# Kernel tuning notes

Measured on AMD Instinct MI355X. Metric: run time of the kernel, lower is better.

The kernel has to match this reference:

```python
import jax, jax.numpy as jnp
import numpy as np

N_NODES, N_EDGES = 16000, 256000
M_IN_S, M_IN_V = 16, 8   # input irreps: 16x0e + 8x1o (dim 40)
M_K_S, M_K_V = 8, 4      # key/query irreps: 8x0e + 4x1o
M_V_S, M_V_V = 16, 8     # value irreps: 16x0e + 8x1o
NUM_BASIS, R_CUT = 32, 2.5
SQ3 = 1.7320508075688772  # sqrt(3)


def _fc_net(r, W1, W2):
    # e3nn FullyConnectedNet([num_basis,16,numels], silu): weight-normalized linears
    h = jax.nn.silu(r @ (W1 / jnp.sqrt(jnp.float32(W1.shape[0]))))
    return h @ (W2 / jnp.sqrt(jnp.float32(W2.shape[0])))


def _edge_tp(xs, xv, y0, y1, w, m1s, m1v, mos, mov):
    # FullyConnectedTensorProduct(in1 = m1s x0e + m1v x1o, in2 = 1x0e + 1x1o,
    #   out = mos x0e + mov x1o), per-edge external weights w [E, numels].
    # Paths: 0e*0e->0e, 1o*1o->0e (dot/sqrt3), 0e*1o->1o, 1o*0e->1o.
    E = w.shape[0]
    n1, n2, n3 = m1s * mos, m1v * mos, m1s * mov
    w_ss = w[:, :n1].reshape(E, m1s, mos)
    w_vv = w[:, n1:n1 + n2].reshape(E, m1v, mos)
    w_sv = w[:, n1 + n2:n1 + n2 + n3].reshape(E, m1s, mov)
    w_vs = w[:, n1 + n2 + n3:].reshape(E, m1v, mov)
    inv = 1.0 / jnp.sqrt(jnp.float32(m1s + m1v))  # fan-in path normalization
    out_s = (jnp.einsum('ei,eio->eo', xs * y0[:, None], w_ss)
             + jnp.einsum('eic,ec,eio->eo', xv, y1, w_vv) / SQ3) * inv
    out_v = (jnp.einsum('ei,ec,eio->eoc', xs, y1, w_sv)
             + jnp.einsum('eic,eio->eoc', xv * y0[:, None, None], w_vs)) * inv
    return out_s, out_v


def _forward(pos, x, Wq_s, Wq_v, Wk1, Wk2, Wv1, Wv2, Ws_ss, Ws_vv, edge_src, edge_dst):
    xs, xv = x[:, :M_IN_S], x[:, M_IN_S:].reshape(-1, M_IN_V, 3)
    vec = pos[edge_dst] - pos[edge_src]                       # [E,3]
    d = jnp.linalg.norm(vec, axis=1)
    d_safe = jnp.maximum(d, 1e-6)
    # bessel radial basis with cutoff (soft_one_hot_linspace, basis='bessel') * sqrt(num_basis)
    n = jnp.arange(1, NUM_BASIS + 1, dtype=jnp.float32)
    rad = jnp.sqrt(2.0 / R_CUT) * jnp.sin(n[None] * jnp.pi * d_safe[:, None] / R_CUT) / d_safe[:, None]
    rad = jnp.where((d < R_CUT)[:, None], rad, 0.0) * jnp.sqrt(jnp.float32(NUM_BASIS))
    # spherical harmonics lmax=1, normalize=True, component normalization
    vh = vec / d_safe[:, None]
    y0, y1 = jnp.ones_like(d), SQ3 * vh
    # query projection (o3.Linear: per-irrep linear with 1/sqrt(fan_in))
    q_s = xs @ Wq_s / jnp.sqrt(jnp.float32(M_IN_S))           # [N, M_K_S]
    q_v = jnp.einsum('nic,io->noc', xv, Wq_v) / jnp.sqrt(jnp.float32(M_IN_V))
    # per-edge tensor-product weights from radial MLPs (shared_weights=False)
    wk = _fc_net(rad, Wk1, Wk2)                               # [E, 288]
    wv = _fc_net(rad, Wv1, Wv2)                               # [E, 576]
    xs_e, xv_e = xs[edge_src], xv[edge_src]
    k_s, k_v = _edge_tp(xs_e, xv_e, y0, y1, wk, M_IN_S, M_IN_V, M_K_S, M_K_V)
    v_s, v_v = _edge_tp(xs_e, xv_e, y0, y1, wv, M_IN_S, M_IN_V, M_V_S, M_V_V)
    # similarity tensor product (query x key -> 0e), shared internal weights
    fan = jnp.sqrt(jnp.float32(M_K_S * M_K_S + M_K_V * M_K_V))
    sim = (jnp.einsum('ei,ij,ej->e', q_s[edge_dst], Ws_ss, k_s)
           + jnp.einsum('eic,ij,ejc->e', q_v[edge_dst], Ws_vv, k_v) / SQ3) / fan
    # scatter softmax over incoming edges of each dst node
    attn = jnp.exp(sim)
    Z = jax.ops.segment_sum(attn, edge_dst, num_segments=N_NODES)
    a = attn / Z[edge_dst]
    # weighted scatter-sum aggregation
    out_s = jax.ops.segment_sum(a[:, None] * v_s, edge_dst, num_segments=N_NODES)
    out_v = jax.ops.segment_sum(a[:, None, None] * v_v, edge_dst, num_segments=N_NODES)
    return jnp.concatenate([out_s, out_v.reshape(N_NODES, -1)], axis=1)  # [N, 40]


def setup_inputs() -> dict:
    key = jax.random.key(0)
    ks = jax.random.split(key, 12)
    wk_numels = M_IN_S * M_K_S + M_IN_V * M_K_S + M_IN_S * M_K_V + M_IN_V * M_K_V  # 288
    wv_numels = M_IN_S * M_V_S + M_IN_V * M_V_S + M_IN_S * M_V_V + M_IN_V * M_V_V  # 576
    return {
        'pos': jax.random.uniform(ks[0], (N_NODES, 3), jnp.float32) * 3.0,
        'x': jax.random.normal(ks[1], (N_NODES, M_IN_S + 3 * M_IN_V), jnp.float32),
        'Wq_s': jax.random.normal(ks[2], (M_IN_S, M_K_S), jnp.float32),
        'Wq_v': jax.random.normal(ks[3], (M_IN_V, M_K_V), jnp.float32),
        'Wk1': jax.random.normal(ks[4], (NUM_BASIS, 16), jnp.float32),
        'Wk2': jax.random.normal(ks[5], (16, wk_numels), jnp.float32),
        'Wv1': jax.random.normal(ks[6], (NUM_BASIS, 16), jnp.float32),
        'Wv2': jax.random.normal(ks[7], (16, wv_numels), jnp.float32),
        'Ws_ss': jax.random.normal(ks[8], (M_K_S, M_K_S), jnp.float32) * 0.1,
        'Ws_vv': jax.random.normal(ks[9], (M_K_V, M_K_V), jnp.float32) * 0.1,
        'edge_src': jax.random.randint(ks[10], (N_EDGES,), 0, N_NODES),
        'edge_dst': jax.random.randint(ks[11], (N_EDGES,), 0, N_NODES),
    }


def reference(pos, x, Wq_s, Wq_v, Wk1, Wk2, Wv1, Wv2, Ws_ss, Ws_vv, edge_src, edge_dst):
    return _forward(pos, x, Wq_s, Wq_v, Wk1, Wk2, Wv1, Wv2, Ws_ss, Ws_vv, edge_src, edge_dst)
```

## Files before the change

kernel.cpp:

```cpp
#include <hip/hip_runtime.h>
#include <hip/hip_bf16.h>

#define N_NODES 16000
#define N_EDGES 256000

#define OFF_SD     0
#define OFF_SIMB   512000
#define OFF_CNT    768000
#define OFF_START  784000
#define OFF_CUR    800001
#define OFF_WB     816004
#define OFF_WBK    834436

typedef _Float16 f16x2 __attribute__((ext_vector_type(2)));
typedef _Float16 f16x8v __attribute__((ext_vector_type(8)));
typedef float f32x4v __attribute__((ext_vector_type(4)));

__device__ __forceinline__ float fdot2f(f16x2 a, f16x2 b, float c) {
#if __has_builtin(__builtin_amdgcn_fdot2)
  return __builtin_amdgcn_fdot2(a, b, c, false);
#else
  return fmaf((float)a.x, (float)b.x, fmaf((float)a.y, (float)b.y, c));
#endif
}

__device__ __forceinline__ unsigned packh2(float a, float b) {
  union { unsigned u; f16x2 p; } v;
  v.p.x = (_Float16)a; v.p.y = (_Float16)b;
  return v.u;
}

__device__ __forceinline__ void load_row40(const float* __restrict__ p, float* xr) {
  const float4* rp = reinterpret_cast<const float4*>(p);
#pragma unroll
  for (int q = 0; q < 10; ++q) {
    float4 f = rp[q];
    xr[4 * q + 0] = f.x; xr[4 * q + 1] = f.y; xr[4 * q + 2] = f.z; xr[4 * q + 3] = f.w;
  }
}

struct EdgeGeom { float vhx, vhy, vhz, y1x, y1y, y1z; };

__device__ __forceinline__ void edge_h_pk(const float* __restrict__ pos, int s, int d,
                                          const unsigned* W1, f16x2* hp, EdgeGeom& g) {
  float vx = pos[3 * d + 0] - pos[3 * s + 0];
  float vy = pos[3 * d + 1] - pos[3 * s + 1];
  float vz = pos[3 * d + 2] - pos[3 * s + 2];
  float dist = sqrtf(fmaf(vx, vx, fmaf(vy, vy, vz * vz)));
  float dsafe = fmaxf(dist, 1e-6f);
  float rinv = 1.0f / dsafe;
  g.vhx = vx * rinv; g.vhy = vy * rinv; g.vhz = vz * rinv;
  g.y1x = 1.7320508075688772f * g.vhx;
  g.y1y = 1.7320508075688772f * g.vhy;
  g.y1z = 1.7320508075688772f * g.vhz;
  float pre[16];
#pragma unroll
  for (int t = 0; t < 16; ++t) pre[t] = 0.f;
  float sx, cx;
  sincosf(1.2566370614359172f * dsafe, &sx, &cx);
  cx = fminf(1.f, fmaxf(-1.f, cx));
  float twoc = 2.f * cx;
  float sprev = 0.f, scur = sx;
  float rscale = (dist < 2.5f) ? (5.059644256269407f * rinv) : 0.f;
#pragma unroll
  for (int bp = 0; bp < 16; ++bp) {
    float r0 = rscale * scur;
    float sn = fmaf(twoc, scur, -sprev); sprev = scur; scur = sn;
    float r1 = rscale * scur;
    sn = fmaf(twoc, scur, -sprev); sprev = scur; scur = sn;
    union { unsigned u; f16x2 p; } rp; rp.p.x = (_Float16)r0; rp.p.y = (_Float16)r1;
    union { uint4 u[4]; f16x2 p[16]; } w;
    w.u[0] = *(const uint4*)(W1 + bp * 16);
    w.u[1] = *(const uint4*)(W1 + bp * 16 + 4);
    w.u[2] = *(const uint4*)(W1 + bp * 16 + 8);
    w.u[3] = *(const uint4*)(W1 + bp * 16 + 12);
#pragma unroll
    for (int t = 0; t < 16; ++t) pre[t] = fdot2f(rp.p, w.p[t], pre[t]);
  }
#pragma unroll
  for (int tp = 0; tp < 8; ++tp) {
    float h0 = pre[2 * tp]     / (1.f + __expf(-pre[2 * tp]));
    float h1 = pre[2 * tp + 1] / (1.f + __expf(-pre[2 * tp + 1]));
    hp[tp].x = (_Float16)h0; hp[tp].y = (_Float16)h1;
  }
}

__global__ void k_hist(const int* __restrict__ edst, int* __restrict__ cnt) {
  int e = blockIdx.x * 256 + threadIdx.x;
  atomicAdd(&cnt[edst[e]], 1);
}

__global__ void __launch_bounds__(1024) k_scan(const int* __restrict__ cnt,
                                               int* __restrict__ start, int* __restrict__ cur) {
  __shared__ int part[1024];
  int t = threadIdx.x;
  int base = t * 16;
  int local[16];
  int sum = 0;
#pragma unroll
  for (int i = 0; i < 16; ++i) {
    int idx = base + i;
    int c = (idx < N_NODES) ? cnt[idx] : 0;
    local[i] = sum; sum += c;
  }
  part[t] = sum;
  __syncthreads();
  for (int off = 1; off < 1024; off <<= 1) {
    int v = (t >= off) ? part[t - off] : 0;
    __syncthreads();
    part[t] += v;
    __syncthreads();
  }
  int prev = (t == 0) ? 0 : part[t - 1];
#pragma unroll
  for (int i = 0; i < 16; ++i) {
    int idx = base + i;
    if (idx < N_NODES) { int st = prev + local[i]; start[idx] = st; cur[idx] = st; }
  }
  if (t == 0) start[N_NODES] = N_EDGES;
}

__global__ void k_fill(const int* __restrict__ esrc, const int* __restrict__ edst,
                       int* __restrict__ cur, int2* __restrict__ sd) {
  int e = blockIdx.x * 256 + threadIdx.x;
  int d = edst[e];
  int slot = atomicAdd(&cur[d], 1);
  sd[slot] = make_int2(esrc[e], d);
}

__global__ void k_prepB(const float* __restrict__ Wv2, unsigned short* __restrict__ WB) {
  int idx = blockIdx.x * 256 + threadIdx.x;
  int j = idx & 7;
  int lane = (idx >> 3) & 63;
  int t3 = idx >> 9;
  int ct = t3 % 3, kk = t3 / 3;
  int q = lane >> 4, m = lane & 15;
  int row = 32 * kk + 8 * q + j;
  int col = 16 * ct + m;
  int t = row & 15;
  float v = 0.f;
  if (row < 256) {
    int i = row >> 4;
    if (col < 16)      v = Wv2[t * 576 + i * 16 + col];
    else if (col < 24) v = Wv2[t * 576 + 384 + i * 8 + (col - 16)];
  } else if (row < 384) {
    int i = (row - 256) >> 4;
    if (col < 16)      v = Wv2[t * 576 + 256 + i * 16 + col];
  } else {
    int part = (row - 384) >> 7;
    int i = ((row - 384) & 127) >> 4;
    int cb = 24 + 8 * part;
    if (col >= cb && col < cb + 8) v = Wv2[t * 576 + 512 + i * 8 + (col - cb)];
  }
  union { unsigned short u; _Float16 h; } cv;
  cv.h = (_Float16)(v * 0.051031036307982884f);
  WB[idx] = cv.u;
}

__global__ void k_prepBK(const float* __restrict__ Wk2, unsigned short* __restrict__ WBK) {
  int idx = blockIdx.x * 256 + threadIdx.x;
  int j = idx & 7;
  int lane = (idx >> 3) & 63;
  int t2 = idx >> 9;
  int ct = t2 & 1, kk = t2 >> 1;
  int q = lane >> 4, m = lane & 15;
  int row = 32 * kk + 8 * q + j;
  int col = 16 * ct + m;
  int t = row & 15;
  float v = 0.f;
  if (col < 24) {
    if (row < 256) {
      int i = row >> 4;
      if (col < 8)       v = Wk2[t * 288 + i * 8 + col];
      else if (col < 12) v = Wk2[t * 288 + 192 + i * 4 + (col - 8)];
    } else if (row < 384) {
      int i = (row - 256) >> 4;
      if (col < 8)       v = Wk2[t * 288 + 128 + i * 8 + col];
    } else {
      int c = (row - 384) >> 7;
      int i = ((row - 384) & 127) >> 4;
      int cb = 12 + 4 * c;
      if (col >= cb && col < cb + 4) v = Wk2[t * 288 + 256 + i * 4 + (col - cb)];
    }
  }
  union { unsigned short u; _Float16 h; } cv;
  cv.h = (_Float16)(v * 0.051031036307982884f);
  WBK[idx] = cv.u;
}

#define ZTW 20

__global__ void __launch_bounds__(256) k_edge1(
    const float* __restrict__ pos, const float* __restrict__ x,
    const float* __restrict__ Wq_s, const float* __restrict__ Wq_v,
    const float* __restrict__ Wk1,
    const float* __restrict__ Wss, const float* __restrict__ Wvv,
    const unsigned short* __restrict__ WBK,
    const int2* __restrict__ sd, float* __restrict__ simb) {
  __shared__ __align__(16) unsigned LW1[256];
  __shared__ float Ls[240];
  __shared__ __align__(16) float SM[4][64 * ZTW];

  for (int i = threadIdx.x; i < 256; i += 256) {
    int bp = i >> 4, t = i & 15;
    LW1[i] = packh2(Wk1[(2 * bp) * 16 + t] * 0.17677669529663687f,
                    Wk1[(2 * bp + 1) * 16 + t] * 0.17677669529663687f);
  }
  for (int i = threadIdx.x; i < 240; i += 256) {
    float v;
    if (i < 128)      v = Wq_s[i] * 0.25f;
    else if (i < 160) v = Wq_v[i - 128] * 0.3535533905932738f;
    else if (i < 224) v = Wss[i - 160] * 0.11180339887498948f;
    else              v = Wvv[i - 224] * 0.06454972243679028f;
    Ls[i] = v;
  }
  __syncthreads();

  int wave = threadIdx.x >> 6, lane = threadIdx.x & 63;
  int q = lane >> 4, m = lane & 15;
  int slot = blockIdx.x * 256 + threadIdx.x;
  int2 e = sd[slot];
  int s = e.x, d = e.y;

  f16x2 hp[8]; EdgeGeom g;
  edge_h_pk(pos, s, d, LW1, hp, g);

  float qts[8], qtv[12];
  {
    float xd[40];
    load_row40(x + 40 * d, xd);
    float qd[8], qvd[12];
#pragma unroll
    for (int o = 0; o < 8; ++o) qd[o] = 0.f;
#pragma unroll
    for (int i = 0; i < 16; ++i)
#pragma unroll
      for (int o = 0; o < 8; ++o) qd[o] = fmaf(xd[i], Ls[8 * i + o], qd[o]);
#pragma unroll
    for (int k = 0; k < 12; ++k) qvd[k] = 0.f;
#pragma unroll
    for (int i = 0; i < 8; ++i)
#pragma unroll
      for (int o = 0; o < 4; ++o)
#pragma unroll
        for (int c = 0; c < 3; ++c)
          qvd[3 * o + c] = fmaf(xd[16 + 3 * i + c], Ls[128 + 4 * i + o], qvd[3 * o + c]);
#pragma unroll
    for (int j = 0; j < 8; ++j) {
      float t = 0.f;
#pragma unroll
      for (int i = 0; i < 8; ++i) t = fmaf(qd[i], Ls[160 + 8 * i + j], t);
      qts[j] = t;
    }
#pragma unroll
    for (int o = 0; o < 4; ++o)
#pragma unroll
      for (int c = 0; c < 3; ++c) {
        float t = 0.f;
#pragma unroll
        for (int i = 0; i < 4; ++i) t = fmaf(qvd[3 * i + c], Ls[224 + 4 * i + o], t);
        qtv[3 * o + c] = t;
      }
  }

  float xr[40];
  load_row40(x + 40 * s, xr);
  float xs[16];
#pragma unroll
  for (int i = 0; i < 16; ++i) xs[i] = xr[i];
  float Bv[8];
#pragma unroll
  for (int i = 0; i < 8; ++i)
    Bv[i] = fmaf(xr[16 + 3 * i], g.vhx, fmaf(xr[17 + 3 * i], g.vhy, xr[18 + 3 * i] * g.vhz));
  f16x2 cxv[3][4];
#pragma unroll
  for (int p = 0; p < 4; ++p)
#pragma unroll
    for (int c = 0; c < 3; ++c) {
      cxv[c][p].x = (_Float16)xr[16 + 3 * (2 * p) + c];
      cxv[c][p].y = (_Float16)xr[16 + 3 * (2 * p + 1) + c];
    }

  unsigned* zt = (unsigned*)&SM[wave][0];
  const uint4* WBq = (const uint4*)WBK;
  f32x4v acc[4][2];
#pragma unroll
  for (int rt = 0; rt < 4; ++rt)
#pragma unroll
    for (int ct = 0; ct < 2; ++ct) { f32x4v z = {0.f, 0.f, 0.f, 0.f}; acc[rt][ct] = z; }

#pragma unroll
  for (int kk = 0; kk < 24; ++kk) {
    f16x2 sp0, sp1;
    if (kk < 8) {
      sp0.x = sp0.y = (_Float16)xs[2 * kk];
      sp1.x = sp1.y = (_Float16)xs[2 * kk + 1];
    } else if (kk < 12) {
      sp0.x = sp0.y = (_Float16)Bv[2 * (kk - 8)];
      sp1.x = sp1.y = (_Float16)Bv[2 * (kk - 8) + 1];
    } else {
      int part = (kk - 12) >> 2, p = (kk - 12) & 3;
      sp0.x = sp0.y = cxv[part][p].x;
      sp1.x = sp1.y = cxv[part][p].y;
    }
    union { uint4 u[4]; f16x2 z[16]; } Z;
#pragma unroll
    for (int t = 0; t < 8; ++t) { Z.z[t] = hp[t] * sp0; Z.z[8 + t] = hp[t] * sp1; }
    uint4* zrow = (uint4*)(zt + lane * ZTW);
    zrow[0] = Z.u[0]; zrow[1] = Z.u[1]; zrow[2] = Z.u[2]; zrow[3] = Z.u[3];
    union { uint4 u; f16x8v v; } af[4];
#pragma unroll
    for (int rt = 0; rt < 4; ++rt)
      af[rt].u = *(const uint4*)(zt + (16 * rt + m) * ZTW + 4 * q);
#pragma unroll
    for (int ct = 0; ct < 2; ++ct) {
      union { uint4 u; f16x8v v; } bf;
      bf.u = WBq[(kk * 2 + ct) * 64 + lane];
#pragma unroll
      for (int rt = 0; rt < 4; ++rt)
        acc[rt][ct] = __builtin_amdgcn_mfma_f32_16x16x32_f16(af[rt].v, bf.v, acc[rt][ct], 0, 0, 0);
    }
  }

  float P[24];
  float* ctb = &SM[wave][0];
#pragma unroll
  for (int rt = 0; rt < 4; ++rt)
#pragma unroll
    for (int r = 0; r < 4; ++r)
      ctb[(16 * rt + 4 * q + r) * ZTW + m] = acc[rt][0][r];
#pragma unroll
  for (int b = 0; b < 4; ++b) {
    float4 f = *(const float4*)(ctb + lane * ZTW + 4 * b);
    P[4 * b] = f.x; P[4 * b + 1] = f.y; P[4 * b + 2] = f.z; P[4 * b + 3] = f.w;
  }
#pragma unroll
  for (int rt = 0; rt < 4; ++rt)
#pragma unroll
    for (int r = 0; r < 4; ++r)
      ctb[(16 * rt + 4 * q + r) * ZTW + m] = acc[rt][1][r];
#pragma unroll
  for (int b = 0; b < 2; ++b) {
    float4 f = *(const float4*)(ctb + lane * ZTW + 4 * b);
    P[16 + 4 * b] = f.x; P[17 + 4 * b] = f.y; P[18 + 4 * b] = f.z; P[19 + 4 * b] = f.w;
  }

  float sim = 0.f;
#pragma unroll
  for (int j = 0; j < 8; ++j) sim = fmaf(qts[j], P[j], sim);
  float y1c[3] = {g.y1x, g.y1y, g.y1z};
#pragma unroll
  for (int o = 0; o < 4; ++o)
#pragma unroll
    for (int c = 0; c < 3; ++c)
      sim = fmaf(qtv[3 * o + c], fmaf(y1c[c], P[8 + o], P[12 + 4 * c + o]), sim);
  simb[slot] = sim;
}

__global__ void k_norm(const int* __restrict__ start, float* __restrict__ simb) {
  int n = blockIdx.x * 256 + threadIdx.x;
  if (n >= N_NODES) return;
  int a = start[n], b = start[n + 1];
  if (a == b) return;
  float m = -3.4e38f;
  for (int j = a; j < b; ++j) m = fmaxf(m, simb[j]);
  float Z = 0.f;
  for (int j = a; j < b; ++j) { float t = __expf(simb[j] - m); simb[j] = t; Z += t; }
  float inv = 1.f / Z;
  for (int j = a; j < b; ++j) simb[j] *= inv;
}

__global__ void __launch_bounds__(256) k_edge2(
    const float* __restrict__ pos, const float* __restrict__ x,
    const float* __restrict__ Wv1, const unsigned short* __restrict__ WB,
    const int2* __restrict__ sd, const float* __restrict__ ab, float* __restrict__ out) {
  __shared__ __align__(16) unsigned LW1[256];
  __shared__ __align__(16) float SM[4][64 * ZTW];

  for (int i = threadIdx.x; i < 256; i += 256) {
    int bp = i >> 4, t = i & 15;
    LW1[i] = packh2(Wv1[(2 * bp) * 16 + t] * 0.17677669529663687f,
                    Wv1[(2 * bp + 1) * 16 + t] * 0.17677669529663687f);
  }
  __syncthreads();

  int wave = threadIdx.x >> 6, lane = threadIdx.x & 63;
  int q = lane >> 4, m = lane & 15;
  int slot = blockIdx.x * 256 + threadIdx.x;
  int2 e = sd[slot];
  int s = e.x, d = e.y;

  bool same[6];
#pragma unroll
  for (int k = 0; k < 6; ++k) {
    int dd = __shfl_down(d, 1 << k, 64);
    same[k] = ((lane + (1 << k)) < 64) && (dd == d);
  }
  int dprev = __shfl_up(d, 1, 64);
  bool head = (lane == 0) || (dprev != d);

  f16x2 hp[8]; EdgeGeom g;
  edge_h_pk(pos, s, d, LW1, hp, g);
  float xr[40];
  load_row40(x + 40 * s, xr);
  float xs[16];
#pragma unroll
  for (int i = 0; i < 16; ++i) xs[i] = xr[i];
  float Bv[8];
#pragma unroll
  for (int i = 0; i < 8; ++i)
    Bv[i] = fmaf(xr[16 + 3 * i], g.vhx, fmaf(xr[17 + 3 * i], g.vhy, xr[18 + 3 * i] * g.vhz));
  f16x2 cxv[3][4];
#pragma unroll
  for (int p = 0; p < 4; ++p)
#pragma unroll
    for (int c = 0; c < 3; ++c) {
      cxv[c][p].x = (_Float16)xr[16 + 3 * (2 * p) + c];
      cxv[c][p].y = (_Float16)xr[16 + 3 * (2 * p + 1) + c];
    }
  float a = ab[slot];

  unsigned* zt = (unsigned*)&SM[wave][0];
  const uint4* WBq = (const uint4*)WB;
  f32x4v acc[4][3];
#pragma unroll
  for (int rt = 0; rt < 4; ++rt)
#pragma unroll
    for (int ct = 0; ct < 3; ++ct) { f32x4v z = {0.f, 0.f, 0.f, 0.f}; acc[rt][ct] = z; }

#pragma unroll
  for (int kk = 0; kk < 24; ++kk) {
    f16x2 sp0, sp1;
    if (kk < 8) {
      sp0.x = sp0.y = (_Float16)xs[2 * kk];
      sp1.x = sp1.y = (_Float16)xs[2 * kk + 1];
    } else if (kk < 12) {
      sp0.x = sp0.y = (_Float16)Bv[2 * (kk - 8)];
      sp1.x = sp1.y = (_Float16)Bv[2 * (kk - 8) + 1];
    } else {
      int part = (kk - 12) >> 2, p = (kk - 12) & 3;
      sp0.x = sp0.y = cxv[part][p].x;
      sp1.x = sp1.y = cxv[part][p].y;
    }
    union { uint4 u[4]; f16x2 z[16]; } Z;
#pragma unroll
    for (int t = 0; t < 8; ++t) { Z.z[t] = hp[t] * sp0; Z.z[8 + t] = hp[t] * sp1; }
    uint4* zrow = (uint4*)(zt + lane * ZTW);
    zrow[0] = Z.u[0]; zrow[1] = Z.u[1]; zrow[2] = Z.u[2]; zrow[3] = Z.u[3];
    union { uint4 u; f16x8v v; } af[4];
#pragma unroll
    for (int rt = 0; rt < 4; ++rt)
      af[rt].u = *(const uint4*)(zt + (16 * rt + m) * ZTW + 4 * q);
#pragma unroll
    for (int ct = 0; ct < 3; ++ct) {
      union { uint4 u; f16x8v v; } bf;
      bf.u = WBq[(kk * 3 + ct) * 64 + lane];
#pragma unroll
      for (int rt = 0; rt < 4; ++rt)
        acc[rt][ct] = __builtin_amdgcn_mfma_f32_16x16x32_f16(af[rt].v, bf.v, acc[rt][ct], 0, 0, 0);
    }
  }

  float* ctb = &SM[wave][0];
  float* op = out + 40 * d;

  {
#pragma unroll
    for (int rt = 0; rt < 4; ++rt)
#pragma unroll
      for (int r = 0; r < 4; ++r)
        ctb[(16 * rt + 4 * q + r) * ZTW + m] = acc[rt][0][r];
    float P0[16];
#pragma unroll
    for (int b = 0; b < 4; ++b) {
      float4 f = *(const float4*)(ctb + lane * ZTW + 4 * b);
      P0[4 * b] = f.x; P0[4 * b + 1] = f.y; P0[4 * b + 2] = f.z; P0[4 * b + 3] = f.w;
    }
#pragma unroll
    for (int o = 0; o < 16; ++o) {
      float v = a * P0[o];
#pragma unroll
      for (int k = 0; k < 6; ++k) {
        float ov = __shfl_down(v, 1 << k, 64);
        v += same[k] ? ov : 0.f;
      }
      if (head) atomicAdd(op + o, v);
    }
  }
  float P1[16], P2[16];
#pragma unroll
  for (int rt = 0; rt < 4; ++rt)
#pragma unroll
    for (int r = 0; r < 4; ++r)
      ctb[(16 * rt + 4 * q + r) * ZTW + m] = acc[rt][1][r];
#pragma unroll
  for (int b = 0; b < 4; ++b) {
    float4 f = *(const float4*)(ctb + lane * ZTW + 4 * b);
    P1[4 * b] = f.x; P1[4 * b + 1] = f.y; P1[4 * b + 2] = f.z; P1[4 * b + 3] = f.w;
  }
#pragma unroll
  for (int rt = 0; rt < 4; ++rt)
#pragma unroll
    for (int r = 0; r < 4; ++r)
      ctb[(16 * rt + 4 * q + r) * ZTW + m] = acc[rt][2][r];
#pragma unroll
  for (int b = 0; b < 4; ++b) {
    float4 f = *(const float4*)(ctb + lane * ZTW + 4 * b);
    P2[4 * b] = f.x; P2[4 * b + 1] = f.y; P2[4 * b + 2] = f.z; P2[4 * b + 3] = f.w;
  }
#pragma unroll
  for (int o = 0; o < 8; ++o) {
    float s1v = P1[o];
    float vc[3];
    vc[0] = a * fmaf(g.y1x, s1v, P1[8 + o]);
    vc[1] = a * fmaf(g.y1y, s1v, P2[o]);
    vc[2] = a * fmaf(g.y1z, s1v, P2[8 + o]);
#pragma unroll
    for (int c = 0; c < 3; ++c) {
      float v = vc[c];
#pragma unroll
      for (int k = 0; k < 6; ++k) {
        float ov = __shfl_down(v, 1 << k, 64);
        v += same[k] ? ov : 0.f;
      }
      if (head) atomicAdd(op + 16 + 3 * o + c, v);
    }
  }
}

extern "C" void kernel_launch(void* const* d_in, const int* in_sizes, int n_in,
                              void* d_out, int out_size, void* d_ws, size_t ws_size,
                              hipStream_t stream) {
  (void)in_sizes; (void)n_in; (void)out_size; (void)ws_size;
  const float* pos  = (const float*)d_in[0];
  const float* x    = (const float*)d_in[1];
  const float* Wq_s = (const float*)d_in[2];
  const float* Wq_v = (const float*)d_in[3];
  const float* Wk1  = (const float*)d_in[4];
  const float* Wk2  = (const float*)d_in[5];
  const float* Wv1  = (const float*)d_in[6];
  const float* Wv2  = (const float*)d_in[7];
  const float* Wss  = (const float*)d_in[8];
  const float* Wvv  = (const float*)d_in[9];
  const int* esrc = (const int*)d_in[10];
  const int* edst = (const int*)d_in[11];
  int*   wsi  = (int*)d_ws;
  float* wsf  = (float*)d_ws;
  float* out  = (float*)d_out;

  int2*  sd    = (int2*)(wsi + OFF_SD);
  float* simb  = wsf + OFF_SIMB;
  int*   cnt   = wsi + OFF_CNT;
  int*   start = wsi + OFF_START;
  int*   cur   = wsi + OFF_CUR;
  unsigned short* WB  = (unsigned short*)(wsf + OFF_WB);
  unsigned short* WBK = (unsigned short*)(wsf + OFF_WBK);

  hipMemsetAsync(cnt, 0, (size_t)N_NODES * sizeof(int), stream);
  hipMemsetAsync(out, 0, (size_t)(N_NODES * 40) * sizeof(float), stream);
  k_prepB<<<144, 256, 0, stream>>>(Wv2, WB);
  k_prepBK<<<96, 256, 0, stream>>>(Wk2, WBK);
  k_hist<<<1000, 256, 0, stream>>>(edst, cnt);
  k_scan<<<1, 1024, 0, stream>>>(cnt, start, cur);
  k_fill<<<1000, 256, 0, stream>>>(esrc, edst, cur, sd);
  k_edge1<<<1000, 256, 0, stream>>>(pos, x, Wq_s, Wq_v, Wk1, Wss, Wvv, WBK, sd, simb);
  k_norm<<<63, 256, 0, stream>>>(start, simb);
  k_edge2<<<1000, 256, 0, stream>>>(pos, x, Wv1, WB, sd, simb, out);
}
```

Baseline: 247.2 us.

## Precompute per-node queries and build MFMA A-operands in registers via splat

Moves the query projection (Wq then Ws) out of the per-edge kernel into a new per-node kernel that writes fp16 queries, so each edge only loads 20 halves instead of recomputing from the 40-float destination row. The per-edge outer-product operand is now built in registers: h and the coefficients are staged once in LDS, and each k-step multiplies the h fragment by a perm-splatted coefficient. This replaces the per-k-step LDS write and readback. The C-tile transpose uses a padded stride-65 layout. Queries are now held in fp16, which costs some precision, and an extra small kernel launch is added.

New measurement: 236.8 us. -4.2%, faster.

```diff
diff --git a/kernel.cpp b/kernel.cpp
--- a/kernel.cpp
+++ b/kernel.cpp
@@ -11,6 +11,7 @@
 #define OFF_CUR    800001
 #define OFF_WB     816004
 #define OFF_WBK    834436
+#define OFF_QT     846724
 
 typedef _Float16 f16x2 __attribute__((ext_vector_type(2)));
 typedef _Float16 f16x8v __attribute__((ext_vector_type(8)));
@@ -28,6 +29,15 @@
   union { unsigned u; f16x2 p; } v;
   v.p.x = (_Float16)a; v.p.y = (_Float16)b;
   return v.u;
+}
+
+__device__ __forceinline__ unsigned splat_half(unsigned x, unsigned sel) {
+#if __has_builtin(__builtin_amdgcn_perm)
+  return __builtin_amdgcn_perm(x, x, sel);
+#else
+  unsigned h = (sel == 0x03020302u) ? (x >> 16) : (x & 0xffffu);
+  return h | (h << 16);
+#endif
 }
 
 __device__ __forceinline__ void load_row40(const float* __restrict__ p, float* xr) {
@@ -188,25 +198,13 @@
   WBK[idx] = cv.u;
 }
 
-#define ZTW 20
-
-__global__ void __launch_bounds__(256) k_edge1(
-    const float* __restrict__ pos, const float* __restrict__ x,
+__global__ void __launch_bounds__(128) k_nodeq(
+    const float* __restrict__ x,
     const float* __restrict__ Wq_s, const float* __restrict__ Wq_v,
-    const float* __restrict__ Wk1,
     const float* __restrict__ Wss, const float* __restrict__ Wvv,
-    const unsigned short* __restrict__ WBK,
-    const int2* __restrict__ sd, float* __restrict__ simb) {
-  __shared__ __align__(16) unsigned LW1[256];
+    unsigned short* __restrict__ QT) {
   __shared__ float Ls[240];
-  __shared__ __align__(16) float SM[4][64 * ZTW];
-
-  for (int i = threadIdx.x; i < 256; i += 256) {
-    int bp = i >> 4, t = i & 15;
-    LW1[i] = packh2(Wk1[(2 * bp) * 16 + t] * 0.17677669529663687f,
-                    Wk1[(2 * bp + 1) * 16 + t] * 0.17677669529663687f);
-  }
-  for (int i = threadIdx.x; i < 240; i += 256) {
+  for (int i = threadIdx.x; i < 240; i += 128) {
     float v;
     if (i < 128)      v = Wq_s[i] * 0.25f;
     else if (i < 160) v = Wq_v[i - 128] * 0.3535533905932738f;
@@ -215,9 +213,87 @@
     Ls[i] = v;
   }
   __syncthreads();
+  int n = blockIdx.x * 128 + threadIdx.x;
+  float xd[40];
+  load_row40(x + 40 * n, xd);
+  float qd[8], qvd[12];
+#pragma unroll
+  for (int o = 0; o < 8; ++o) qd[o] = 0.f;
+#pragma unroll
+  for (int i = 0; i < 16; ++i)
+#pragma unroll
+    for (int o = 0; o < 8; ++o) qd[o] = fmaf(xd[i], Ls[8 * i + o], qd[o]);
+#pragma unroll
+  for (int k = 0; k < 12; ++k) qvd[k] = 0.f;
+#pragma unroll
+  for (int i = 0; i < 8; ++i)
+#pragma unroll
+    for (int o = 0; o < 4; ++o)
+#pragma unroll
+      for (int c = 0; c < 3; ++c)
+        qvd[3 * o + c] = fmaf(xd[16 + 3 * i + c], Ls[128 + 4 * i + o], qvd[3 * o + c]);
+  float qf[20];
+#pragma unroll
+  for (int j = 0; j < 8; ++j) {
+    float t = 0.f;
+#pragma unroll
+    for (int i = 0; i < 8; ++i) t = fmaf(qd[i], Ls[160 + 8 * i + j], t);
+    qf[j] = t;
+  }
+#pragma unroll
+  for (int o = 0; o < 4; ++o)
+#pragma unroll
+    for (int c = 0; c < 3; ++c) {
+      float t = 0.f;
+#pragma unroll
+      for (int i = 0; i < 4; ++i) t = fmaf(qvd[3 * i + c], Ls[224 + 4 * i + o], t);
+      qf[8 + 3 * o + c] = t;
+    }
+  uint2* qp = (uint2*)(QT + 20 * n);
+#pragma unroll
+  for (int b = 0; b < 5; ++b) {
+    uint2 st;
+    st.x = packh2(qf[4 * b], qf[4 * b + 1]);
+    st.y = packh2(qf[4 * b + 2], qf[4 * b + 3]);
+    qp[b] = st;
+  }
+}
+
+#define RSTR 36
+
+__device__ __forceinline__ void build_coef(const float* xr, const float* Bv, float* coef) {
+#pragma unroll
+  for (int i = 0; i < 16; ++i) coef[i] = xr[i];
+#pragma unroll
+  for (int i = 0; i < 8; ++i) coef[16 + i] = Bv[i];
+#pragma unroll
+  for (int p = 0; p < 4; ++p)
+#pragma unroll
+    for (int c = 0; c < 3; ++c) {
+      coef[24 + 8 * c + 2 * p]     = xr[16 + 6 * p + c];
+      coef[24 + 8 * c + 2 * p + 1] = xr[16 + 6 * p + 3 + c];
+    }
+}
+
+__global__ void __launch_bounds__(256) k_edge1(
+    const float* __restrict__ pos, const float* __restrict__ x,
+    const float* __restrict__ Wk1, const unsigned short* __restrict__ WBK,
+    const unsigned short* __restrict__ QT,
+    const int2* __restrict__ sd, float* __restrict__ simb) {
+  __shared__ __align__(16) unsigned LW1[256];
+  __shared__ __align__(16) unsigned SM[4][64 * RSTR];
+
+  for (int i = threadIdx.x; i < 256; i += 256) {
+    int bp = i >> 4, t = i & 15;
+    LW1[i] = packh2(Wk1[(2 * bp) * 16 + t] * 0.17677669529663687f,
+                    Wk1[(2 * bp + 1) * 16 + t] * 0.17677669529663687f);
+  }
+  __syncthreads();
 
   int wave = threadIdx.x >> 6, lane = threadIdx.x & 63;
   int q = lane >> 4, m = lane & 15;
+  int q1 = q & 1;
+  unsigned seld = (q >> 1) ? 0x03020302u : 0x01000100u;
   int slot = blockIdx.x * 256 + threadIdx.x;
   int2 e = sd[slot];
   int s = e.x, d = e.y;
@@ -225,63 +301,51 @@
   f16x2 hp[8]; EdgeGeom g;
   edge_h_pk(pos, s, d, LW1, hp, g);
 
-  float qts[8], qtv[12];
+  float qf[20];
   {
-    float xd[40];
-    load_row40(x + 40 * d, xd);
-    float qd[8], qvd[12];
-#pragma unroll
-    for (int o = 0; o < 8; ++o) qd[o] = 0.f;
-#pragma unroll
-    for (int i = 0; i < 16; ++i)
-#pragma unroll
-      for (int o = 0; o < 8; ++o) qd[o] = fmaf(xd[i], Ls[8 * i + o], qd[o]);
-#pragma unroll
-    for (int k = 0; k < 12; ++k) qvd[k] = 0.f;
-#pragma unroll
-    for (int i = 0; i < 8; ++i)
-#pragma unroll
-      for (int o = 0; o < 4; ++o)
-#pragma unroll
-        for (int c = 0; c < 3; ++c)
-          qvd[3 * o + c] = fmaf(xd[16 + 3 * i + c], Ls[128 + 4 * i + o], qvd[3 * o + c]);
-#pragma unroll
-    for (int j = 0; j < 8; ++j) {
-      float t = 0.f;
-#pragma unroll
-      for (int i = 0; i < 8; ++i) t = fmaf(qd[i], Ls[160 + 8 * i + j], t);
-      qts[j] = t;
-    }
-#pragma unroll
-    for (int o = 0; o < 4; ++o)
-#pragma unroll
-      for (int c = 0; c < 3; ++c) {
-        float t = 0.f;
-#pragma unroll
-        for (int i = 0; i < 4; ++i) t = fmaf(qvd[3 * i + c], Ls[224 + 4 * i + o], t);
-        qtv[3 * o + c] = t;
-      }
+    const uint2* qp = (const uint2*)(QT + 20 * d);
+#pragma unroll
+    for (int b = 0; b < 5; ++b) {
+      uint2 u = qp[b];
+      union { unsigned d; f16x2 p; } a0, a1;
+      a0.d = u.x; a1.d = u.y;
+      qf[4 * b] = (float)a0.p.x; qf[4 * b + 1] = (float)a0.p.y;
+      qf[4 * b + 2] = (float)a1.p.x; qf[4 * b + 3] = (float)a1.p.y;
+    }
   }
 
   float xr[40];
   load_row40(x + 40 * s, xr);
-  float xs[16];
-#pragma unroll
-  for (int i = 0; i < 16; ++i) xs[i] = xr[i];
   float Bv[8];
 #pragma unroll
   for (int i = 0; i < 8; ++i)
     Bv[i] = fmaf(xr[16 + 3 * i], g.vhx, fmaf(xr[17 + 3 * i], g.vhy, xr[18 + 3 * i] * g.vhz));
-  f16x2 cxv[3][4];
-#pragma unroll
-  for (int p = 0; p < 4; ++p)
-#pragma unroll
-    for (int c = 0; c < 3; ++c) {
-      cxv[c][p].x = (_Float16)xr[16 + 3 * (2 * p) + c];
-      cxv[c][p].y = (_Float16)xr[16 + 3 * (2 * p + 1) + c];
-    }
-
-  unsigned* zt = (unsigned*)&SM[wave][0];
+  float coef[48];
+  build_coef(xr, Bv, coef);
+
+  unsigned* row = &SM[wave][lane * RSTR];
+  {
+    union { uint4 u; f16x2 p[4]; } h0, h1;
+#pragma unroll
+    for (int k = 0; k < 4; ++k) { h0.p[k] = hp[k]; h1.p[k] = hp[4 + k]; }
+    *(uint4*)(row) = h0.u;
+    *(uint4*)(row + 4) = h1.u;
+  }
+#pragma unroll
+  for (int bt = 0; bt < 6; ++bt) {
+    uint4 w;
+    w.x = packh2(coef[8 * bt + 0], coef[8 * bt + 1]);
+    w.y = packh2(coef[8 * bt + 2], coef[8 * bt + 3]);
+    w.z = packh2(coef[8 * bt + 4], coef[8 * bt + 5]);
+    w.w = packh2(coef[8 * bt + 6], coef[8 * bt + 7]);
+    *(uint4*)(row + 8 + 4 * bt) = w;
+  }
+  unsigned* wbase = &SM[wave][0];
+  union { uint4 u; f16x2 p[4]; } hs[4];
+#pragma unroll
+  for (int rt = 0; rt < 4; ++rt)
+    hs[rt].u = *(const uint4*)(wbase + (16 * rt + m) * RSTR + 4 * q1);
+
   const uint4* WBq = (const uint4*)WBK;
   f32x4v acc[4][2];
 #pragma unroll
@@ -290,70 +354,59 @@
     for (int ct = 0; ct < 2; ++ct) { f32x4v z = {0.f, 0.f, 0.f, 0.f}; acc[rt][ct] = z; }
 
 #pragma unroll
-  for (int kk = 0; kk < 24; ++kk) {
-    f16x2 sp0, sp1;
-    if (kk < 8) {
-      sp0.x = sp0.y = (_Float16)xs[2 * kk];
-      sp1.x = sp1.y = (_Float16)xs[2 * kk + 1];
-    } else if (kk < 12) {
-      sp0.x = sp0.y = (_Float16)Bv[2 * (kk - 8)];
-      sp1.x = sp1.y = (_Float16)Bv[2 * (kk - 8) + 1];
-    } else {
-      int part = (kk - 12) >> 2, p = (kk - 12) & 3;
-      sp0.x = sp0.y = cxv[part][p].x;
-      sp1.x = sp1.y = cxv[part][p].y;
-    }
-    union { uint4 u[4]; f16x2 z[16]; } Z;
-#pragma unroll
-    for (int t = 0; t < 8; ++t) { Z.z[t] = hp[t] * sp0; Z.z[8 + t] = hp[t] * sp1; }
-    uint4* zrow = (uint4*)(zt + lane * ZTW);
-    zrow[0] = Z.u[0]; zrow[1] = Z.u[1]; zrow[2] = Z.u[2]; zrow[3] = Z.u[3];
-    union { uint4 u; f16x8v v; } af[4];
+  for (int bt = 0; bt < 6; ++bt) {
+    union { uint4 u; unsigned d[4]; } cb[4];
 #pragma unroll
     for (int rt = 0; rt < 4; ++rt)
-      af[rt].u = *(const uint4*)(zt + (16 * rt + m) * ZTW + 4 * q);
-#pragma unroll
-    for (int ct = 0; ct < 2; ++ct) {
-      union { uint4 u; f16x8v v; } bf;
-      bf.u = WBq[(kk * 2 + ct) * 64 + lane];
-#pragma unroll
-      for (int rt = 0; rt < 4; ++rt)
-        acc[rt][ct] = __builtin_amdgcn_mfma_f32_16x16x32_f16(af[rt].v, bf.v, acc[rt][ct], 0, 0, 0);
+      cb[rt].u = *(const uint4*)(wbase + (16 * rt + m) * RSTR + 8 + 4 * bt);
+#pragma unroll
+    for (int t = 0; t < 4; ++t) {
+      int kk = 4 * bt + t;
+      union { uint4 u; f16x2 p[4]; f16x8v v; } av[4];
+#pragma unroll
+      for (int rt = 0; rt < 4; ++rt) {
+        union { unsigned d; f16x2 p; } sp;
+        sp.d = splat_half(cb[rt].d[t], seld);
+#pragma unroll
+        for (int w = 0; w < 4; ++w) av[rt].p[w] = hs[rt].p[w] * sp.p;
+      }
+#pragma unroll
+      for (int ct = 0; ct < 2; ++ct) {
+        union { uint4 u; f16x8v v; } bf;
+        bf.u = WBq[(kk * 2 + ct) * 64 + lane];
+#pragma unroll
+        for (int rt = 0; rt < 4; ++rt)
+          acc[rt][ct] = __builtin_amdgcn_mfma_f32_16x16x32_f16(av[rt].v, bf.v, acc[rt][ct], 0, 0, 0);
+      }
     }
   }
 
   float P[24];
-  float* ctb = &SM[wave][0];
+  float* ctb = (float*)wbase;
 #pragma unroll
   for (int rt = 0; rt < 4; ++rt)
 #pragma unroll
     for (int r = 0; r < 4; ++r)
-      ctb[(16 * rt + 4 * q + r) * ZTW + m] = acc[rt][0][r];
-#pragma unroll
-  for (int b = 0; b < 4; ++b) {
-    float4 f = *(const float4*)(ctb + lane * ZTW + 4 * b);
-    P[4 * b] = f.x; P[4 * b + 1] = f.y; P[4 * b + 2] = f.z; P[4 * b + 3] = f.w;
-  }
+      ctb[m * 65 + 16 * rt + 4 * q + r] = acc[rt][0][r];
+#pragma unroll
+  for (int o = 0; o < 16; ++o) P[o] = ctb[o * 65 + lane];
 #pragma unroll
   for (int rt = 0; rt < 4; ++rt)
 #pragma unroll
     for (int r = 0; r < 4; ++r)
-      ctb[(16 * rt + 4 * q + r) * ZTW + m] = acc[rt][1][r];
-#pragma unroll
-  for (int b = 0; b < 2; ++b) {
-    float4 f = *(const float4*)(ctb + lane * ZTW + 4 * b);
-    P[16 + 4 * b] = f.x; P[17 + 4 * b] = f.y; P[18 + 4 * b] = f.z; P[19 + 4 * b] = f.w;
-  }
+      ctb[m * 65 + 16 * rt + 4 * q + r] = acc[rt][1][r];
+#pragma unroll
+  for (int o = 0; o < 8; ++o) P[16 + o] = ctb[o * 65 + lane];
 
   float sim = 0.f;
 #pragma unroll
-  for (int j = 0; j < 8; ++j) sim = fmaf(qts[j], P[j], sim);
+  for (int j = 0; j < 8; ++j) sim = fmaf(qf[j], P[j], sim);
   float y1c[3] = {g.y1x, g.y1y, g.y1z};
 #pragma unroll
   for (int o = 0; o < 4; ++o)
 #pragma unroll
     for (int c = 0; c < 3; ++c)
-      sim = fmaf(qtv[3 * o + c], fmaf(y1c[c], P[8 + o], P[12 + 4 * c + o]), sim);
+      sim = fmaf(qf[8 + 3 * o + c], fmaf(y1c[c], P[8 + o], P[12 + 4 * c + o]), sim);
   simb[slot] = sim;
 }
 
@@ -375,7 +428,7 @@
     const float* __restrict__ Wv1, const unsigned short* __restrict__ WB,
     const int2* __restrict__ sd, const float* __restrict__ ab, float* __restrict__ out) {
   __shared__ __align__(16) unsigned LW1[256];
-  __shared__ __align__(16) float SM[4][64 * ZTW];
+  __shared__ __align__(16) unsigned SM[4][64 * RSTR];
 
   for (int i = threadIdx.x; i < 256; i += 256) {
     int bp = i >> 4, t = i & 15;
@@ -386,6 +439,8 @@
 
   int wave = threadIdx.x >> 6, lane = threadIdx.x & 63;
   int q = lane >> 4, m = lane & 15;
+  int q1 = q & 1;
+  unsigned seld = (q >> 1) ? 0x03020302u : 0x01000100u;
   int slot = blockIdx.x * 256 + threadIdx.x;
   int2 e = sd[slot];
   int s = e.x, d = e.y;
@@ -403,24 +458,37 @@
   edge_h_pk(pos, s, d, LW1, hp, g);
   float xr[40];
   load_row40(x + 40 * s, xr);
-  float xs[16];
-#pragma unroll
-  for (int i = 0; i < 16; ++i) xs[i] = xr[i];
   float Bv[8];
 #pragma unroll
   for (int i = 0; i < 8; ++i)
     Bv[i] = fmaf(xr[16 + 3 * i], g.vhx, fmaf(xr[17 + 3 * i], g.vhy, xr[18 + 3 * i] * g.vhz));
-  f16x2 cxv[3][4];
-#pragma unroll
-  for (int p = 0; p < 4; ++p)
-#pragma unroll
-    for (int c = 0; c < 3; ++c) {
-      cxv[c][p].x = (_Float16)xr[16 + 3 * (2 * p) + c];
-      cxv[c][p].y = (_Float16)xr[16 + 3 * (2 * p + 1) + c];
-    }
+  float coef[48];
+  build_coef(xr, Bv, coef);
   float a = ab[slot];
 
-  unsigned* zt = (unsigned*)&SM[wave][0];
+  unsigned* row = &SM[wave][lane * RSTR];
+  {
+    union { uint4 u; f16x2 p[4]; } h0, h1;
+#pragma unroll
+    for (int k = 0; k < 4; ++k) { h0.p[k] = hp[k]; h1.p[k] = hp[4 + k]; }
+    *(uint4*)(row) = h0.u;
+    *(uint4*)(row + 4) = h1.u;
+  }
+#pragma unroll
+  for (int bt = 0; bt < 6; ++bt) {
+    uint4 w;
+    w.x = packh2(coef[8 * bt + 0], coef[8 * bt + 1]);
+    w.y = packh2(coef[8 * bt + 2], coef[8 * bt + 3]);
+    w.z = packh2(coef[8 * bt + 4], coef[8 * bt + 5]);
+    w.w = packh2(coef[8 * bt + 6], coef[8 * bt + 7]);
+    *(uint4*)(row + 8 + 4 * bt) = w;
+  }
+  unsigned* wbase = &SM[wave][0];
+  union { uint4 u; f16x2 p[4]; } hs[4];
+#pragma unroll
+  for (int rt = 0; rt < 4; ++rt)
+    hs[rt].u = *(const uint4*)(wbase + (16 * rt + m) * RSTR + 4 * q1);
+
   const uint4* WBq = (const uint4*)WB;
   f32x4v acc[4][3];
 #pragma unroll
@@ -429,39 +497,34 @@
     for (int ct = 0; ct < 3; ++ct) { f32x4v z = {0.f, 0.f, 0.f, 0.f}; acc[rt][ct] = z; }
 
 #pragma unroll
-  for (int kk = 0; kk < 24; ++kk) {
-    f16x2 sp0, sp1;
-    if (kk < 8) {
-      sp0.x = sp0.y = (_Float16)xs[2 * kk];
-      sp1.x = sp1.y = (_Float16)xs[2 * kk + 1];
-    } else if (kk < 12) {
-      sp0.x = sp0.y = (_Float16)Bv[2 * (kk - 8)];
-      sp1.x = sp1.y = (_Float16)Bv[2 * (kk - 8) + 1];
-    } else {
-      int part = (kk - 12) >> 2, p = (kk - 12) & 3;
-      sp0.x = sp0.y = cxv[part][p].x;
-      sp1.x = sp1.y = cxv[part][p].y;
-    }
-    union { uint4 u[4]; f16x2 z[16]; } Z;
-#pragma unroll
-    for (int t = 0; t < 8; ++t) { Z.z[t] = hp[t] * sp0; Z.z[8 + t] = hp[t] * sp1; }
-    uint4* zrow = (uint4*)(zt + lane * ZTW);
-    zrow[0] = Z.u[0]; zrow[1] = Z.u[1]; zrow[2] = Z.u[2]; zrow[3] = Z.u[3];
-    union { uint4 u; f16x8v v; } af[4];
+  for (int bt = 0; bt < 6; ++bt) {
+    union { uint4 u; unsigned d[4]; } cb[4];
 #pragma unroll
     for (int rt = 0; rt < 4; ++rt)
-      af[rt].u = *(const uint4*)(zt + (16 * rt + m) * ZTW + 4 * q);
-#pragma unroll
-    for (int ct = 0; ct < 3; ++ct) {
-      union { uint4 u; f16x8v v; } bf;
-      bf.u = WBq[(kk * 3 + ct) * 64 + lane];
-#pragma unroll
-      for (int rt = 0; rt < 4; ++rt)
-        acc[rt][ct] = __builtin_amdgcn_mfma_f32_16x16x32_f16(af[rt].v, bf.v, acc[rt][ct], 0, 0, 0);
-    }
-  }
-
-  float* ctb = &SM[wave][0];
+      cb[rt].u = *(const uint4*)(wbase + (16 * rt + m) * RSTR + 8 + 4 * bt);
+#pragma unroll
+    for (int t = 0; t < 4; ++t) {
+      int kk = 4 * bt + t;
+      union { uint4 u; f16x2 p[4]; f16x8v v; } av[4];
+#pragma unroll
+      for (int rt = 0; rt < 4; ++rt) {
+        union { unsigned d; f16x2 p; } sp;
+        sp.d = splat_half(cb[rt].d[t], seld);
+#pragma unroll
+        for (int w = 0; w < 4; ++w) av[rt].p[w] = hs[rt].p[w] * sp.p;
+      }
+#pragma unroll
+      for (int ct = 0; ct < 3; ++ct) {
+        union { uint4 u; f16x8v v; } bf;
+        bf.u = WBq[(kk * 3 + ct) * 64 + lane];
+#pragma unroll
+        for (int rt = 0; rt < 4; ++rt)
+          acc[rt][ct] = __builtin_amdgcn_mfma_f32_16x16x32_f16(av[rt].v, bf.v, acc[rt][ct], 0, 0, 0);
+      }
+    }
+  }
+
+  float* ctb = (float*)wbase;
   float* op = out + 40 * d;
 
   {
@@ -469,13 +532,10 @@
     for (int rt = 0; rt < 4; ++rt)
 #pragma unroll
       for (int r = 0; r < 4; ++r)
-        ctb[(16 * rt + 4 * q + r) * ZTW + m] = acc[rt][0][r];
+        ctb[m * 65 + 16 * rt + 4 * q + r] = acc[rt][0][r];
     float P0[16];
 #pragma unroll
-    for (int b = 0; b < 4; ++b) {
-      float4 f = *(const float4*)(ctb + lane * ZTW + 4 * b);
-      P0[4 * b] = f.x; P0[4 * b + 1] = f.y; P0[4 * b + 2] = f.z; P0[4 * b + 3] = f.w;
-    }
+    for (int o = 0; o < 16; ++o) P0[o] = ctb[o * 65 + lane];
 #pragma unroll
     for (int o = 0; o < 16; ++o) {
       float v = a * P0[o];
@@ -492,22 +552,16 @@
   for (int rt = 0; rt < 4; ++rt)
 #pragma unroll
     for (int r = 0; r < 4; ++r)
-      ctb[(16 * rt + 4 * q + r) * ZTW + m] = acc[rt][1][r];
-#pragma unroll
-  for (int b = 0; b < 4; ++b) {
-    float4 f = *(const float4*)(ctb + lane * ZTW + 4 * b);
-    P1[4 * b] = f.x; P1[4 * b + 1] = f.y; P1[4 * b + 2] = f.z; P1[4 * b + 3] = f.w;
-  }
+      ctb[m * 65 + 16 * rt + 4 * q + r] = acc[rt][1][r];
+#pragma unroll
+  for (int o = 0; o < 16; ++o) P1[o] = ctb[o * 65 + lane];
 #pragma unroll
   for (int rt = 0; rt < 4; ++rt)
 #pragma unroll
     for (int r = 0; r < 4; ++r)
-      ctb[(16 * rt + 4 * q + r) * ZTW + m] = acc[rt][2][r];
-#pragma unroll
-  for (int b = 0; b < 4; ++b) {
-    float4 f = *(const float4*)(ctb + lane * ZTW + 4 * b);
-    P2[4 * b] = f.x; P2[4 * b + 1] = f.y; P2[4 * b + 2] = f.z; P2[4 * b + 3] = f.w;
-  }
+      ctb[m * 65 + 16 * rt + 4 * q + r] = acc[rt][2][r];
+#pragma unroll
+  for (int o = 0; o < 16; ++o) P2[o] = ctb[o * 65 + lane];
 #pragma unroll
   for (int o = 0; o < 8; ++o) {
     float s1v = P1[o];
@@ -555,15 +609,17 @@
   int*   cur   = wsi + OFF_CUR;
   unsigned short* WB  = (unsigned short*)(wsf + OFF_WB);
   unsigned short* WBK = (unsigned short*)(wsf + OFF_WBK);
+  unsigned short* QT  = (unsigned short*)(wsf + OFF_QT);
 
   hipMemsetAsync(cnt, 0, (size_t)N_NODES * sizeof(int), stream);
   hipMemsetAsync(out, 0, (size_t)(N_NODES * 40) * sizeof(float), stream);
   k_prepB<<<144, 256, 0, stream>>>(Wv2, WB);
   k_prepBK<<<96, 256, 0, stream>>>(Wk2, WBK);
+  k_nodeq<<<125, 128, 0, stream>>>(x, Wq_s, Wq_v, Wss, Wvv, QT);
   k_hist<<<1000, 256, 0, stream>>>(edst, cnt);
   k_scan<<<1, 1024, 0, stream>>>(cnt, start, cur);
   k_fill<<<1000, 256, 0, stream>>>(esrc, edst, cur, sd);
-  k_edge1<<<1000, 256, 0, stream>>>(pos, x, Wq_s, Wq_v, Wk1, Wss, Wvv, WBK, sd, simb);
+  k_edge1<<<1000, 256, 0, stream>>>(pos, x, Wk1, WBK, QT, sd, simb);
   k_norm<<<63, 256, 0, stream>>>(start, simb);
   k_edge2<<<1000, 256, 0, stream>>>(pos, x, Wv1, WB, sd, simb, out);
 }
```
